# Optimization experiments

Measured on AMD Instinct MI355X. Metric: run time of the kernel, lower is better.

## Reference

```python
import jax, jax.numpy as jnp
import numpy as np

B, N, F, D, H, T = 32, 1024, 32, 64, 64, 4


def setup_inputs() -> dict:
    key = jax.random.key(0)
    ks = jax.random.split(key, 12)
    def w(k, shape):
        return 0.01 * jax.random.normal(k, shape, dtype=jnp.float32)
    z = lambda *s: jnp.zeros(s, jnp.float32)
    return {
        "xv": jax.random.normal(ks[0], (B, N, F), dtype=jnp.float32),
        "option": jax.random.uniform(ks[1], (B, 1), dtype=jnp.float32),
        "adj": jax.random.normal(ks[2], (N, N), dtype=jnp.float32),
        "mu1": w(ks[3], (F, D)),
        "W2": w(ks[4], (D, D)), "b2": z(D),
        "W3": w(ks[5], (D, D)), "b3": z(D),
        "W4": w(ks[6], (D, 1)), "b4": z(D),
        "Wq1": w(ks[7], (D, D)), "bq1": z(D),
        "Wq2": w(ks[8], (D, 1)), "bq2": z(D),
        "Wreg": w(ks[9], (H, 2 * D)), "breg": z(H),
        "Wq": w(ks[10], (1, H)), "bq": z(1),
    }


def reference(xv, option, adj, mu1, W2, b2, W3, b3, W4, b4,
              Wq1, bq1, Wq2, bq2, Wreg, breg, Wq, bq):
    # binary adjacency for message passing, raw weights for the mu_4 branch
    A = (adj > 0).astype(xv.dtype)                       # [N,N]
    mu_1 = jnp.maximum(xv @ mu1, 0.0)                    # [B,N,D]
    # mu_4: Linear(1,D) over every edge weight, clamp, sum over neighbors
    # (identical value every round t>=1, so computed once)
    mu4 = jnp.maximum(adj[..., None] * W4[:, 0] + b4, 0.0).sum(axis=1)[None]  # [1,N,D]
    mu3 = mu4 @ W3.T + b3                                # [1,N,D]
    mu = mu_1                                            # t = 0
    for _ in range(1, T):                                # t = 1..T-1
        mu_pool = jnp.einsum('nm,bmd->bnd', A, mu)       # neighbor aggregation
        mu2 = mu_pool @ W2.T + b2
        mu = jnp.maximum(mu_1 + mu2 + mu3, 0.0)
    mu_mean = jnp.maximum(mu.mean(axis=1, keepdims=True) @ Wq1.T + bq1, 0.0)  # [B,1,D]
    mu_aug = jnp.concatenate([mu, mu_mean], axis=1)      # [B,N+1,D]
    q2 = option.reshape(B, 1, 1) @ Wq2.T + bq2           # [B,1,D]
    q2 = jnp.broadcast_to(q2, (B, N + 1, D))
    q_ = jnp.concatenate([mu_aug, q2], axis=-1)          # [B,N+1,2D]
    qreg = jnp.maximum(q_ @ Wreg.T + breg, 0.0)          # [B,N+1,H]
    return qreg @ Wq.T + bq                              # [B,N+1,1]
```

## Files before the change

kernel.cpp:

```cpp
#include <hip/hip_runtime.h>
#include <hip/hip_bf16.h>

#define Bc 32
#define Nc 1024
#define Fc 32
#define Dc 64
#define Hc 64

typedef __bf16 bf16;
typedef __bf16 bf16x4 __attribute__((ext_vector_type(4)));
typedef __bf16 bf16x8 __attribute__((ext_vector_type(8)));
typedef float  f32x4  __attribute__((ext_vector_type(4)));

#define MS 72
#define LDS_RND_NONF 18432
#define LDS_RND_FIN  37376


__global__ void k_init(const float* __restrict__ adj, const float* __restrict__ W4,
                       const float* __restrict__ b4, const float* __restrict__ W3,
                       const float* __restrict__ b3, const float* __restrict__ b2,
                       const float* __restrict__ W2, const float* __restrict__ option,
                       const float* __restrict__ Wq2, const float* __restrict__ bq2,
                       const float* __restrict__ Wreg, const float* __restrict__ breg,
                       const float* __restrict__ xv, const float* __restrict__ mu1w,
                       bf16* __restrict__ Afrag, float* __restrict__ C3,
                       bf16* __restrict__ W2bf, float* __restrict__ c2base,
                       float* __restrict__ musum,
                       float* __restrict__ mu_1, bf16* __restrict__ Xfrag0) {
    const int id = blockIdx.x, t = threadIdx.x;
    __shared__ char smem[39424];
    if (id < 1024) {
        const int n = id;
        float* red   = (float*)smem;
        float* mu4_s = red + 256;
        const float* arow = adj + (size_t)n * Nc;
        {
            const int m0 = t * 4;
            const float4 a = *(const float4*)&arow[m0];
            bf16x4 o;
            o[0] = (bf16)((a.x > 0.f) ? 1.f : 0.f);
            o[1] = (bf16)((a.y > 0.f) ? 1.f : 0.f);
            o[2] = (bf16)((a.z > 0.f) ? 1.f : 0.f);
            o[3] = (bf16)((a.w > 0.f) ? 1.f : 0.f);
            const int g = n >> 4, lm = n & 15;
            const int k0 = m0 >> 5, q = (m0 & 31) >> 3, j = m0 & 7;
            *(bf16x4*)&Afrag[(size_t)((g * 32 + k0) * 64 + lm + 16 * q) * 8 + j] = o;
        }
        const int e = t & 63, g = t >> 6;
        const float w4e = W4[e], b4e = b4[e];
        float acc = 0.f;
        const float4* arow4 = (const float4*)(arow + g * 256);
#pragma unroll 8
        for (int j = 0; j < 64; ++j) {
            const float4 av = arow4[j];
            acc += fmaxf(fmaf(av.x, w4e, b4e), 0.f);
            acc += fmaxf(fmaf(av.y, w4e, b4e), 0.f);
            acc += fmaxf(fmaf(av.z, w4e, b4e), 0.f);
            acc += fmaxf(fmaf(av.w, w4e, b4e), 0.f);
        }
        red[t] = acc;
        __syncthreads();
        if (g == 0) mu4_s[e] = red[e] + red[64 + e] + red[128 + e] + red[192 + e];
        __syncthreads();
        if (t < 64) {
            const int d = t;
            float a = b3[d] + b2[d];
#pragma unroll
            for (int ee = 0; ee < 64; ++ee) a = fmaf(mu4_s[ee], W3[d * 64 + ee], a);
            C3[n * 64 + d] = a;
        }
    } else if (id == 1024) {
        for (int j = t * 16; j < t * 16 + 16; ++j) W2bf[j] = (bf16)W2[j];
        for (int i = t; i < 2048; i += 256) musum[i] = 0.f;
        for (int i = t; i < 2048; i += 256) {
            const int b = i >> 6, h = i & 63;
            const float opt = option[b];
            float a = breg[h];
#pragma unroll
            for (int j = 0; j < 64; ++j)
                a = fmaf(fmaf(opt, Wq2[j], bq2[j]), Wreg[h * 128 + 64 + j], a);
            c2base[i] = a;
        }
    } else {
        const int idx = id - 1025, nb = idx & 15, b = idx >> 4;
        const int n0 = nb * 64;
        const int l = t & 63, wv = t >> 6, lm = l & 15, q = l >> 4;
        bf16* W2s = (bf16*)smem;
        bf16* xhi = (bf16*)(smem + 9216);
        bf16* xlo = (bf16*)(smem + 14336);
        bf16* whi = (bf16*)(smem + 19456);
        bf16* wlo = (bf16*)(smem + 24576);
        bf16* muS = (bf16*)(smem + 29696);
        {
            const int row = t >> 2, f0 = (t & 3) * 8;
            const float* src = &xv[((size_t)b * Nc + n0 + row) * Fc + f0];
            const float4 v0 = *(const float4*)src;
            const float4 v1 = *(const float4*)(src + 4);
            bf16x8 hi, lo;
            float vv[8] = {v0.x, v0.y, v0.z, v0.w, v1.x, v1.y, v1.z, v1.w};
#pragma unroll
            for (int j = 0; j < 8; ++j) { hi[j] = (bf16)vv[j]; lo[j] = (bf16)(vv[j] - (float)hi[j]); }
            *(bf16x8*)&xhi[row * 40 + f0] = hi;
            *(bf16x8*)&xlo[row * 40 + f0] = lo;
        }
        {
            const int d = t >> 2, f0 = (t & 3) * 8;
#pragma unroll
            for (int j = 0; j < 8; ++j) {
                const float v = mu1w[(f0 + j) * Dc + d];
                const bf16 hi = (bf16)v;
                whi[d * 40 + f0 + j] = hi;
                wlo[d * 40 + f0 + j] = (bf16)(v - (float)hi);
            }
        }
        {
            const int row = t >> 2, c0 = (t & 3) * 16;
            const float4 v0 = *(const float4*)&W2[row * 64 + c0];
            const float4 v1 = *(const float4*)&W2[row * 64 + c0 + 4];
            const float4 v2 = *(const float4*)&W2[row * 64 + c0 + 8];
            const float4 v3 = *(const float4*)&W2[row * 64 + c0 + 12];
            bf16x8 p0, p1;
            p0[0]=(bf16)v0.x; p0[1]=(bf16)v0.y; p0[2]=(bf16)v0.z; p0[3]=(bf16)v0.w;
            p0[4]=(bf16)v1.x; p0[5]=(bf16)v1.y; p0[6]=(bf16)v1.z; p0[7]=(bf16)v1.w;
            p1[0]=(bf16)v2.x; p1[1]=(bf16)v2.y; p1[2]=(bf16)v2.z; p1[3]=(bf16)v2.w;
            p1[4]=(bf16)v3.x; p1[5]=(bf16)v3.y; p1[6]=(bf16)v3.z; p1[7]=(bf16)v3.w;
            *(bf16x8*)&W2s[row * MS + c0] = p0;
            *(bf16x8*)&W2s[row * MS + c0 + 8] = p1;
        }
        __syncthreads();
        f32x4 acc[4];
#pragma unroll
        for (int ct = 0; ct < 4; ++ct)
#pragma unroll
            for (int r = 0; r < 4; ++r) acc[ct][r] = 0.f;
        {
            const bf16x8 aHi = *(const bf16x8*)&xhi[(wv * 16 + lm) * 40 + q * 8];
            const bf16x8 aLo = *(const bf16x8*)&xlo[(wv * 16 + lm) * 40 + q * 8];
#pragma unroll
            for (int ct = 0; ct < 4; ++ct) {
                const bf16x8 bHi = *(const bf16x8*)&whi[(ct * 16 + lm) * 40 + q * 8];
                const bf16x8 bLo = *(const bf16x8*)&wlo[(ct * 16 + lm) * 40 + q * 8];
                acc[ct] = __builtin_amdgcn_mfma_f32_16x16x32_bf16(aHi, bHi, acc[ct], 0, 0, 0);
                acc[ct] = __builtin_amdgcn_mfma_f32_16x16x32_bf16(aLo, bHi, acc[ct], 0, 0, 0);
                acc[ct] = __builtin_amdgcn_mfma_f32_16x16x32_bf16(aHi, bLo, acc[ct], 0, 0, 0);
            }
        }
#pragma unroll
        for (int ct = 0; ct < 4; ++ct) {
            const int col = ct * 16 + lm;
#pragma unroll
            for (int r = 0; r < 4; ++r) {
                const int row = wv * 16 + q * 4 + r;
                const float v = fmaxf(acc[ct][r], 0.f);
                mu_1[((size_t)b * Nc + n0 + row) * Dc + col] = v;
                muS[row * MS + col] = (bf16)v;
            }
        }
        __syncthreads();
        f32x4 xacc[4];
#pragma unroll
        for (int ct = 0; ct < 4; ++ct)
#pragma unroll
            for (int r = 0; r < 4; ++r) xacc[ct][r] = 0.f;
#pragma unroll
        for (int s = 0; s < 2; ++s) {
            bf16x8 a = *(const bf16x8*)&muS[(wv * 16 + lm) * MS + s * 32 + q * 8];
#pragma unroll
            for (int ct = 0; ct < 4; ++ct) {
                bf16x8 bv = *(const bf16x8*)&W2s[(ct * 16 + lm) * MS + s * 32 + q * 8];
                xacc[ct] = __builtin_amdgcn_mfma_f32_16x16x32_bf16(a, bv, xacc[ct], 0, 0, 0);
            }
        }
        const int k0 = nb * 2 + (wv >> 1);
        const int q_c = (wv & 1) * 2 + (q >> 1);
        const int j0 = (q & 1) * 4;
#pragma unroll
        for (int ct = 0; ct < 4; ++ct) {
            bf16x4 p;
#pragma unroll
            for (int r = 0; r < 4; ++r) p[r] = (bf16)xacc[ct][r];
            *(bf16x4*)&Xfrag0[(size_t)b * 65536
                              + (size_t)((ct * 32 + k0) * 64 + lm + 16 * q_c) * 8 + j0] = p;
        }
    }
}

template <bool FINAL>
__global__ __launch_bounds__(256, 2)
void k_round(const bf16* __restrict__ Afrag, const bf16* __restrict__ Xfr_in,
             const float* __restrict__ mu_1, const float* __restrict__ C3,
             const bf16* __restrict__ W2bf, bf16* __restrict__ Xfr_out,
             const float* __restrict__ Wreg, const float* __restrict__ c2base,
             const float* __restrict__ Wq, const float* __restrict__ bq,
             float* __restrict__ musum, float* __restrict__ out) {
    const int b = blockIdx.x, nb = blockIdx.y, t = threadIdx.x;
    const int n0 = nb * 64;
    const int l = t & 63, wv = t >> 6, lm = l & 15, q = l >> 4;
    const int rh = wv & 1, ch = wv >> 1;
    extern __shared__ char smem[];
    bf16* muHi = (bf16*)smem;
    bf16* muLo = (bf16*)(smem + 9216);
    bf16* WHi  = (bf16*)(smem + (FINAL ? 18432 : 9216));
    bf16* WLo  = (bf16*)(smem + 27648);
    float* rpart = (float*)(smem + 36864);

    if (!FINAL) {
#pragma unroll
        for (int i = 0; i < 2; ++i) {
            int g = i * 256 + t, row = g >> 3, c = g & 7;
            *(bf16x8*)&WHi[row * MS + c * 8] = *(const bf16x8*)&W2bf[row * 64 + c * 8];
        }
    } else {
#pragma unroll
        for (int i = 0; i < 4; ++i) {
            int g = i * 1024 + t * 4, h = g >> 6, d = g & 63;
            const float4 w4 = *(const float4*)&Wreg[h * 128 + d];
            bf16x4 ohi, olo;
            ohi[0] = (bf16)w4.x; olo[0] = (bf16)(w4.x - (float)ohi[0]);
            ohi[1] = (bf16)w4.y; olo[1] = (bf16)(w4.y - (float)ohi[1]);
            ohi[2] = (bf16)w4.z; olo[2] = (bf16)(w4.z - (float)ohi[2]);
            ohi[3] = (bf16)w4.w; olo[3] = (bf16)(w4.w - (float)ohi[3]);
            *(bf16x4*)&WHi[h * MS + d] = ohi;
            *(bf16x4*)&WLo[h * MS + d] = olo;
        }
    }

    f32x4 acc[2][2];
#pragma unroll
    for (int rt = 0; rt < 2; ++rt)
#pragma unroll
        for (int ct = 0; ct < 2; ++ct)
#pragma unroll
            for (int r = 0; r < 4; ++r) acc[rt][ct][r] = 0.f;

    const int gA = nb * 4 + rh * 2;
    const bf16* pa0 = Afrag + (size_t)(gA + 0) * 32 * 512 + l * 8;
    const bf16* pa1 = Afrag + (size_t)(gA + 1) * 32 * 512 + l * 8;
    const bf16* px0 = Xfr_in + (size_t)b * 65536 + (size_t)(ch * 2 + 0) * 32 * 512 + l * 8;
    const bf16* px1 = Xfr_in + (size_t)b * 65536 + (size_t)(ch * 2 + 1) * 32 * 512 + l * 8;
#pragma unroll 4
    for (int k0 = 0; k0 < 32; ++k0) {
        const int o = k0 * 512;
        bf16x8 a0 = *(const bf16x8*)&pa0[o];
        bf16x8 a1 = *(const bf16x8*)&pa1[o];
        bf16x8 x0 = *(const bf16x8*)&px0[o];
        bf16x8 x1 = *(const bf16x8*)&px1[o];
        acc[0][0] = __builtin_amdgcn_mfma_f32_16x16x32_bf16(a0, x0, acc[0][0], 0, 0, 0);
        acc[0][1] = __builtin_amdgcn_mfma_f32_16x16x32_bf16(a0, x1, acc[0][1], 0, 0, 0);
        acc[1][0] = __builtin_amdgcn_mfma_f32_16x16x32_bf16(a1, x0, acc[1][0], 0, 0, 0);
        acc[1][1] = __builtin_amdgcn_mfma_f32_16x16x32_bf16(a1, x1, acc[1][1], 0, 0, 0);
    }

    float vals[2][2][4];
#pragma unroll
    for (int rt = 0; rt < 2; ++rt)
#pragma unroll
        for (int ct = 0; ct < 2; ++ct) {
            const int col = ch * 32 + ct * 16 + lm;
#pragma unroll
            for (int r = 0; r < 4; ++r) {
                const int n = n0 + rh * 32 + rt * 16 + q * 4 + r;
                float v = mu_1[((size_t)b * Nc + n) * Dc + col] + acc[rt][ct][r]
                        + C3[n * 64 + col];
                vals[rt][ct][r] = fmaxf(v, 0.f);
            }
        }

#pragma unroll
    for (int rt = 0; rt < 2; ++rt)
#pragma unroll
        for (int ct = 0; ct < 2; ++ct) {
            const int col = ch * 32 + ct * 16 + lm;
#pragma unroll
            for (int r = 0; r < 4; ++r) {
                const int row = rh * 32 + rt * 16 + q * 4 + r;
                const float v = vals[rt][ct][r];
                const bf16 hi = (bf16)v;
                muHi[row * MS + col] = hi;
                if (FINAL) muLo[row * MS + col] = (bf16)(v - (float)hi);
            }
        }
    if (FINAL) {
#pragma unroll
        for (int ct = 0; ct < 2; ++ct) {
            float s = 0.f;
#pragma unroll
            for (int rt = 0; rt < 2; ++rt)
#pragma unroll
                for (int r = 0; r < 4; ++r) s += vals[rt][ct][r];
            s += __shfl_xor(s, 16);
            s += __shfl_xor(s, 32);
            if (q == 0) atomicAdd(&musum[b * 64 + ch * 32 + ct * 16 + lm], s);
        }
    }
    __syncthreads();

    f32x4 xacc[2][2];
#pragma unroll
    for (int rt = 0; rt < 2; ++rt)
#pragma unroll
        for (int ct = 0; ct < 2; ++ct)
#pragma unroll
            for (int r = 0; r < 4; ++r) xacc[rt][ct][r] = 0.f;

    if (!FINAL) {
#pragma unroll
        for (int s = 0; s < 2; ++s) {
            bf16x8 aM[2], bW[2];
#pragma unroll
            for (int rt = 0; rt < 2; ++rt)
                aM[rt] = *(const bf16x8*)&muHi[(rh * 32 + rt * 16 + lm) * MS + s * 32 + q * 8];
#pragma unroll
            for (int ct = 0; ct < 2; ++ct)
                bW[ct] = *(const bf16x8*)&WHi[(ch * 32 + ct * 16 + lm) * MS + s * 32 + q * 8];
#pragma unroll
            for (int rt = 0; rt < 2; ++rt)
#pragma unroll
                for (int ct = 0; ct < 2; ++ct)
                    xacc[rt][ct] = __builtin_amdgcn_mfma_f32_16x16x32_bf16(aM[rt], bW[ct],
                                                                           xacc[rt][ct], 0, 0, 0);
        }
        const int k0 = nb * 2 + rh;
        const int q_c0 = (q >> 1), j0 = (q & 1) * 4;
#pragma unroll
        for (int rt = 0; rt < 2; ++rt)
#pragma unroll
            for (int ct = 0; ct < 2; ++ct) {
                bf16x4 p;
#pragma unroll
                for (int r = 0; r < 4; ++r) p[r] = (bf16)xacc[rt][ct][r];
                *(bf16x4*)&Xfr_out[(size_t)b * 65536
                    + (size_t)(((ch * 2 + ct) * 32 + k0) * 64 + lm + 16 * (rt * 2 + q_c0)) * 8
                    + j0] = p;
            }
    } else {
#pragma unroll
        for (int s = 0; s < 2; ++s) {
            bf16x8 aH[2], aL[2], bH[2], bL[2];
#pragma unroll
            for (int rt = 0; rt < 2; ++rt) {
                const int ao = (rh * 32 + rt * 16 + lm) * MS + s * 32 + q * 8;
                aH[rt] = *(const bf16x8*)&muHi[ao];
                aL[rt] = *(const bf16x8*)&muLo[ao];
            }
#pragma unroll
            for (int ct = 0; ct < 2; ++ct) {
                const int bo = (ch * 32 + ct * 16 + lm) * MS + s * 32 + q * 8;
                bH[ct] = *(const bf16x8*)&WHi[bo];
                bL[ct] = *(const bf16x8*)&WLo[bo];
            }
#pragma unroll
            for (int rt = 0; rt < 2; ++rt)
#pragma unroll
                for (int ct = 0; ct < 2; ++ct) {
                    xacc[rt][ct] = __builtin_amdgcn_mfma_f32_16x16x32_bf16(aH[rt], bH[ct],
                                                                           xacc[rt][ct], 0, 0, 0);
                    xacc[rt][ct] = __builtin_amdgcn_mfma_f32_16x16x32_bf16(aL[rt], bH[ct],
                                                                           xacc[rt][ct], 0, 0, 0);
                    xacc[rt][ct] = __builtin_amdgcn_mfma_f32_16x16x32_bf16(aH[rt], bL[ct],
                                                                           xacc[rt][ct], 0, 0, 0);
                }
        }
        const float bq0 = bq[0];
        float rowsum[2][4] = {{0.f, 0.f, 0.f, 0.f}, {0.f, 0.f, 0.f, 0.f}};
#pragma unroll
        for (int ct = 0; ct < 2; ++ct) {
            const int h = ch * 32 + ct * 16 + lm;
            const float c2 = c2base[b * 64 + h];
            const float wqh = Wq[h];
#pragma unroll
            for (int rt = 0; rt < 2; ++rt)
#pragma unroll
                for (int r = 0; r < 4; ++r)
                    rowsum[rt][r] += fmaxf(xacc[rt][ct][r] + c2, 0.f) * wqh;
        }
#pragma unroll
        for (int rt = 0; rt < 2; ++rt)
#pragma unroll
            for (int r = 0; r < 4; ++r) {
                float v = rowsum[rt][r];
                v += __shfl_xor(v, 1);
                v += __shfl_xor(v, 2);
                v += __shfl_xor(v, 4);
                v += __shfl_xor(v, 8);
                if (lm == 0) rpart[ch * 64 + rh * 32 + rt * 16 + q * 4 + r] = v;
            }
        __syncthreads();
        if (t < 64)
            out[(size_t)b * (Nc + 1) + n0 + t] = rpart[t] + rpart[64 + t] + bq0;
    }
}

__global__ void k_tail(const float* __restrict__ musum, const float* __restrict__ Wq1,
                       const float* __restrict__ bq1, const float* __restrict__ Wreg,
                       const float* __restrict__ c2base, const float* __restrict__ Wq,
                       const float* __restrict__ bq, float* __restrict__ out) {
    const int b = blockIdx.x, l = threadIdx.x;
    __shared__ float mean_s[64];
    __shared__ float mp[64];
    mean_s[l] = musum[b * 64 + l] * (1.f / Nc);
    __syncthreads();
    float a = bq1[l];
#pragma unroll
    for (int e = 0; e < 64; ++e) a = fmaf(mean_s[e], Wq1[l * 64 + e], a);
    mp[l] = fmaxf(a, 0.f);
    __syncthreads();
    float h = c2base[b * 64 + l];
#pragma unroll
    for (int d = 0; d < 64; ++d) h = fmaf(mp[d], Wreg[l * 128 + d], h);
    float v = fmaxf(h, 0.f) * Wq[l];
#pragma unroll
    for (int off = 32; off; off >>= 1) v += __shfl_down(v, off);
    if (l == 0) out[(size_t)b * (Nc + 1) + Nc] = v + bq[0];
}

extern "C" void kernel_launch(void* const* d_in, const int* in_sizes, int n_in,
                              void* d_out, int out_size, void* d_ws, size_t ws_size,
                              hipStream_t stream) {
    const float* xv     = (const float*)d_in[0];
    const float* option = (const float*)d_in[1];
    const float* adj    = (const float*)d_in[2];
    const float* mu1w   = (const float*)d_in[3];
    const float* W2     = (const float*)d_in[4];
    const float* b2     = (const float*)d_in[5];
    const float* W3     = (const float*)d_in[6];
    const float* b3     = (const float*)d_in[7];
    const float* W4     = (const float*)d_in[8];
    const float* b4     = (const float*)d_in[9];
    const float* Wq1    = (const float*)d_in[10];
    const float* bq1    = (const float*)d_in[11];
    const float* Wq2    = (const float*)d_in[12];
    const float* bq2    = (const float*)d_in[13];
    const float* Wreg   = (const float*)d_in[14];
    const float* breg   = (const float*)d_in[15];
    const float* Wq     = (const float*)d_in[16];
    const float* bq     = (const float*)d_in[17];
    float* out = (float*)d_out;

    float* ws = (float*)d_ws;
    const size_t MU = (size_t)Bc * Nc * Dc;
    float* mu_1     = ws;
    float* C3       = ws + MU;
    float* c2base   = C3 + 65536;
    float* musum    = c2base + 2048;
    bf16*  Afrag    = (bf16*)(musum + 2048);
    bf16*  W2bf     = Afrag + (size_t)Nc * Nc;
    bf16*  Xf0      = W2bf + 4096;
    bf16*  Xf1      = Xf0 + MU;

    k_init<<<1537, 256, 0, stream>>>(adj, W4, b4, W3, b3, b2, W2, option, Wq2, bq2,
                                     Wreg, breg, xv, mu1w,
                                     Afrag, C3, W2bf, c2base, musum, mu_1, Xf0);
    k_round<false><<<dim3(Bc, 16), 256, LDS_RND_NONF, stream>>>(
        Afrag, Xf0, mu_1, C3, W2bf, Xf1,
        nullptr, nullptr, nullptr, nullptr, nullptr, nullptr);
    k_round<false><<<dim3(Bc, 16), 256, LDS_RND_NONF, stream>>>(
        Afrag, Xf1, mu_1, C3, W2bf, Xf0,
        nullptr, nullptr, nullptr, nullptr, nullptr, nullptr);
    k_round<true><<<dim3(Bc, 16), 256, LDS_RND_FIN, stream>>>(
        Afrag, Xf0, mu_1, C3, nullptr, nullptr,
        Wreg, c2base, Wq, bq, musum, out);
    k_tail<<<Bc, 64, 0, stream>>>(musum, Wq1, bq1, Wreg, c2base, Wq, bq, out);
}
```

Baseline: 153.0 us.

## Double-buffer MFMA operand loads and fold tail into final round via ticket

The k-loop of the round kernel now prefetches the next group of four A/X fragments into registers while running MFMAs on the current group. The mu_1 and C3 epilogue operands are loaded before the loop so their latency is hidden. The separate tail kernel is removed: the last block per batch, chosen by an atomic ticket counter, computes the mean-path output. This saves a launch, but it raises register pressure under launch bounds and relies on threadfence/atomic ordering.

Result: slower. 184.4 us (+20.5%).

```diff
diff --git a/kernel.cpp b/kernel.cpp
--- a/kernel.cpp
+++ b/kernel.cpp
@@ -26,7 +26,7 @@
                        const float* __restrict__ xv, const float* __restrict__ mu1w,
                        bf16* __restrict__ Afrag, float* __restrict__ C3,
                        bf16* __restrict__ W2bf, float* __restrict__ c2base,
-                       float* __restrict__ musum,
+                       float* __restrict__ musum, int* __restrict__ ticket,
                        float* __restrict__ mu_1, bf16* __restrict__ Xfrag0) {
     const int id = blockIdx.x, t = threadIdx.x;
     __shared__ char smem[39424];
@@ -73,6 +73,7 @@
     } else if (id == 1024) {
         for (int j = t * 16; j < t * 16 + 16; ++j) W2bf[j] = (bf16)W2[j];
         for (int i = t; i < 2048; i += 256) musum[i] = 0.f;
+        if (t < 32) ticket[t] = 0;
         for (int i = t; i < 2048; i += 256) {
             const int b = i >> 6, h = i & 63;
             const float opt = option[b];
@@ -193,7 +194,9 @@
              const bf16* __restrict__ W2bf, bf16* __restrict__ Xfr_out,
              const float* __restrict__ Wreg, const float* __restrict__ c2base,
              const float* __restrict__ Wq, const float* __restrict__ bq,
-             float* __restrict__ musum, float* __restrict__ out) {
+             const float* __restrict__ Wq1, const float* __restrict__ bq1,
+             float* __restrict__ musum, int* __restrict__ ticket,
+             float* __restrict__ out) {
     const int b = blockIdx.x, nb = blockIdx.y, t = threadIdx.x;
     const int n0 = nb * 64;
     const int l = t & 63, wv = t >> 6, lm = l & 15, q = l >> 4;
@@ -239,20 +242,17 @@
     const bf16* pa1 = Afrag + (size_t)(gA + 1) * 32 * 512 + l * 8;
     const bf16* px0 = Xfr_in + (size_t)b * 65536 + (size_t)(ch * 2 + 0) * 32 * 512 + l * 8;
     const bf16* px1 = Xfr_in + (size_t)b * 65536 + (size_t)(ch * 2 + 1) * 32 * 512 + l * 8;
-#pragma unroll 4
-    for (int k0 = 0; k0 < 32; ++k0) {
-        const int o = k0 * 512;
-        bf16x8 a0 = *(const bf16x8*)&pa0[o];
-        bf16x8 a1 = *(const bf16x8*)&pa1[o];
-        bf16x8 x0 = *(const bf16x8*)&px0[o];
-        bf16x8 x1 = *(const bf16x8*)&px1[o];
-        acc[0][0] = __builtin_amdgcn_mfma_f32_16x16x32_bf16(a0, x0, acc[0][0], 0, 0, 0);
-        acc[0][1] = __builtin_amdgcn_mfma_f32_16x16x32_bf16(a0, x1, acc[0][1], 0, 0, 0);
-        acc[1][0] = __builtin_amdgcn_mfma_f32_16x16x32_bf16(a1, x0, acc[1][0], 0, 0, 0);
-        acc[1][1] = __builtin_amdgcn_mfma_f32_16x16x32_bf16(a1, x1, acc[1][1], 0, 0, 0);
+
+    bf16x8 bA0[2][4], bA1[2][4], bX0[2][4], bX1[2][4];
+#pragma unroll
+    for (int i = 0; i < 4; ++i) {
+        const int o = i * 512;
+        bA0[0][i] = *(const bf16x8*)&pa0[o];
+        bA1[0][i] = *(const bf16x8*)&pa1[o];
+        bX0[0][i] = *(const bf16x8*)&px0[o];
+        bX1[0][i] = *(const bf16x8*)&px1[o];
     }
-
-    float vals[2][2][4];
+    float pmu[2][2][4], pc3[2][2][4];
 #pragma unroll
     for (int rt = 0; rt < 2; ++rt)
 #pragma unroll
@@ -261,11 +261,42 @@
 #pragma unroll
             for (int r = 0; r < 4; ++r) {
                 const int n = n0 + rh * 32 + rt * 16 + q * 4 + r;
-                float v = mu_1[((size_t)b * Nc + n) * Dc + col] + acc[rt][ct][r]
-                        + C3[n * 64 + col];
-                vals[rt][ct][r] = fmaxf(v, 0.f);
-            }
-        }
+                pmu[rt][ct][r] = mu_1[((size_t)b * Nc + n) * Dc + col];
+                pc3[rt][ct][r] = C3[n * 64 + col];
+            }
+        }
+
+#pragma unroll
+    for (int g = 0; g < 8; ++g) {
+        const int cur = g & 1, nxt = cur ^ 1;
+        if (g < 7) {
+            const int o0 = (g + 1) * 4 * 512;
+#pragma unroll
+            for (int i = 0; i < 4; ++i) {
+                const int o = o0 + i * 512;
+                bA0[nxt][i] = *(const bf16x8*)&pa0[o];
+                bA1[nxt][i] = *(const bf16x8*)&pa1[o];
+                bX0[nxt][i] = *(const bf16x8*)&px0[o];
+                bX1[nxt][i] = *(const bf16x8*)&px1[o];
+            }
+        }
+#pragma unroll
+        for (int i = 0; i < 4; ++i) {
+            acc[0][0] = __builtin_amdgcn_mfma_f32_16x16x32_bf16(bA0[cur][i], bX0[cur][i], acc[0][0], 0, 0, 0);
+            acc[0][1] = __builtin_amdgcn_mfma_f32_16x16x32_bf16(bA0[cur][i], bX1[cur][i], acc[0][1], 0, 0, 0);
+            acc[1][0] = __builtin_amdgcn_mfma_f32_16x16x32_bf16(bA1[cur][i], bX0[cur][i], acc[1][0], 0, 0, 0);
+            acc[1][1] = __builtin_amdgcn_mfma_f32_16x16x32_bf16(bA1[cur][i], bX1[cur][i], acc[1][1], 0, 0, 0);
+        }
+    }
+
+    float vals[2][2][4];
+#pragma unroll
+    for (int rt = 0; rt < 2; ++rt)
+#pragma unroll
+        for (int ct = 0; ct < 2; ++ct)
+#pragma unroll
+            for (int r = 0; r < 4; ++r)
+                vals[rt][ct][r] = fmaxf(pmu[rt][ct][r] + acc[rt][ct][r] + pc3[rt][ct][r], 0.f);
 
 #pragma unroll
     for (int rt = 0; rt < 2; ++rt)
@@ -389,30 +420,34 @@
         __syncthreads();
         if (t < 64)
             out[(size_t)b * (Nc + 1) + n0 + t] = rpart[t] + rpart[64 + t] + bq0;
+
+        __threadfence();
+        __shared__ int lastFlag;
+        if (t == 0) lastFlag = (atomicAdd(&ticket[b], 1) == 15) ? 1 : 0;
+        __syncthreads();
+        if (lastFlag) {
+            float* mean_s = (float*)smem;
+            float* mp     = mean_s + 64;
+            if (t < 64) mean_s[t] = atomicAdd(&musum[b * 64 + t], 0.f) * (1.f / Nc);
+            __syncthreads();
+            if (t < 64) {
+                float a = bq1[t];
+#pragma unroll
+                for (int e = 0; e < 64; ++e) a = fmaf(mean_s[e], Wq1[t * 64 + e], a);
+                mp[t] = fmaxf(a, 0.f);
+            }
+            __syncthreads();
+            if (t < 64) {
+                float h = c2base[b * 64 + t];
+#pragma unroll
+                for (int d = 0; d < 64; ++d) h = fmaf(mp[d], Wreg[t * 128 + d], h);
+                float v = fmaxf(h, 0.f) * Wq[t];
+#pragma unroll
+                for (int off = 32; off; off >>= 1) v += __shfl_down(v, off);
+                if (t == 0) out[(size_t)b * (Nc + 1) + Nc] = v + bq0;
+            }
+        }
     }
-}
-
-__global__ void k_tail(const float* __restrict__ musum, const float* __restrict__ Wq1,
-                       const float* __restrict__ bq1, const float* __restrict__ Wreg,
-                       const float* __restrict__ c2base, const float* __restrict__ Wq,
-                       const float* __restrict__ bq, float* __restrict__ out) {
-    const int b = blockIdx.x, l = threadIdx.x;
-    __shared__ float mean_s[64];
-    __shared__ float mp[64];
-    mean_s[l] = musum[b * 64 + l] * (1.f / Nc);
-    __syncthreads();
-    float a = bq1[l];
-#pragma unroll
-    for (int e = 0; e < 64; ++e) a = fmaf(mean_s[e], Wq1[l * 64 + e], a);
-    mp[l] = fmaxf(a, 0.f);
-    __syncthreads();
-    float h = c2base[b * 64 + l];
-#pragma unroll
-    for (int d = 0; d < 64; ++d) h = fmaf(mp[d], Wreg[l * 128 + d], h);
-    float v = fmaxf(h, 0.f) * Wq[l];
-#pragma unroll
-    for (int off = 32; off; off >>= 1) v += __shfl_down(v, off);
-    if (l == 0) out[(size_t)b * (Nc + 1) + Nc] = v + bq[0];
 }
 
 extern "C" void kernel_launch(void* const* d_in, const int* in_sizes, int n_in,
@@ -444,22 +479,22 @@
     float* C3       = ws + MU;
     float* c2base   = C3 + 65536;
     float* musum    = c2base + 2048;
-    bf16*  Afrag    = (bf16*)(musum + 2048);
+    int*   ticket   = (int*)(musum + 2048);
+    bf16*  Afrag    = (bf16*)(ticket + 64);
     bf16*  W2bf     = Afrag + (size_t)Nc * Nc;
     bf16*  Xf0      = W2bf + 4096;
     bf16*  Xf1      = Xf0 + MU;
 
     k_init<<<1537, 256, 0, stream>>>(adj, W4, b4, W3, b3, b2, W2, option, Wq2, bq2,
                                      Wreg, breg, xv, mu1w,
-                                     Afrag, C3, W2bf, c2base, musum, mu_1, Xf0);
+                                     Afrag, C3, W2bf, c2base, musum, ticket, mu_1, Xf0);
     k_round<false><<<dim3(Bc, 16), 256, LDS_RND_NONF, stream>>>(
         Afrag, Xf0, mu_1, C3, W2bf, Xf1,
-        nullptr, nullptr, nullptr, nullptr, nullptr, nullptr);
+        nullptr, nullptr, nullptr, nullptr, nullptr, nullptr, nullptr, nullptr, nullptr);
     k_round<false><<<dim3(Bc, 16), 256, LDS_RND_NONF, stream>>>(
         Afrag, Xf1, mu_1, C3, W2bf, Xf0,
-        nullptr, nullptr, nullptr, nullptr, nullptr, nullptr);
+        nullptr, nullptr, nullptr, nullptr, nullptr, nullptr, nullptr, nullptr, nullptr);
     k_round<true><<<dim3(Bc, 16), 256, LDS_RND_FIN, stream>>>(
         Afrag, Xf0, mu_1, C3, nullptr, nullptr,
-        Wreg, c2base, Wq, bq, musum, out);
-    k_tail<<<Bc, 64, 0, stream>>>(musum, Wq1, bq1, Wreg, c2base, Wq, bq, out);
+        Wreg, c2base, Wq, bq, Wq1, bq1, musum, ticket, out);
 }
```

## Halve row tile per block in round kernel to double grid and occupancy

Applied to the files above, without the earlier changes.

Each round block now handles 32 node rows instead of 64, so the grid doubles to 32x32 blocks and each wave computes a single 16-row tile. The aim is to fill more CUs and raise occupancy (launch bounds raised to 4 blocks per SM, smaller LDS). mu_1 and C3 epilogue operands are prefetched before the aggregation loop so their latency overlaps with the MFMAs. In exchange, the per-block MFMA work drops and the X fragments are reloaded from memory by twice as many blocks, which adds global/L2 traffic.

Result: slower. 159.8 us (+4.5%).

```diff
diff --git a/kernel.cpp b/kernel.cpp
--- a/kernel.cpp
+++ b/kernel.cpp
@@ -13,8 +13,8 @@
 typedef float  f32x4  __attribute__((ext_vector_type(4)));
 
 #define MS 72
-#define LDS_RND_NONF 18432
-#define LDS_RND_FIN  37376
+#define LDS_RND_NONF 13824
+#define LDS_RND_FIN  27904
 
 
 __global__ void k_init(const float* __restrict__ adj, const float* __restrict__ W4,
@@ -187,7 +187,7 @@
 }
 
 template <bool FINAL>
-__global__ __launch_bounds__(256, 2)
+__global__ __launch_bounds__(256, 4)
 void k_round(const bf16* __restrict__ Afrag, const bf16* __restrict__ Xfr_in,
              const float* __restrict__ mu_1, const float* __restrict__ C3,
              const bf16* __restrict__ W2bf, bf16* __restrict__ Xfr_out,
@@ -195,15 +195,15 @@
              const float* __restrict__ Wq, const float* __restrict__ bq,
              float* __restrict__ musum, float* __restrict__ out) {
     const int b = blockIdx.x, nb = blockIdx.y, t = threadIdx.x;
-    const int n0 = nb * 64;
+    const int n0 = nb * 32;
     const int l = t & 63, wv = t >> 6, lm = l & 15, q = l >> 4;
     const int rh = wv & 1, ch = wv >> 1;
     extern __shared__ char smem[];
     bf16* muHi = (bf16*)smem;
-    bf16* muLo = (bf16*)(smem + 9216);
-    bf16* WHi  = (bf16*)(smem + (FINAL ? 18432 : 9216));
-    bf16* WLo  = (bf16*)(smem + 27648);
-    float* rpart = (float*)(smem + 36864);
+    bf16* muLo = (bf16*)(smem + 4608);
+    bf16* WHi  = (bf16*)(smem + (FINAL ? 9216 : 4608));
+    bf16* WLo  = (bf16*)(smem + 18432);
+    float* rpart = (float*)(smem + 27648);
 
     if (!FINAL) {
 #pragma unroll
@@ -226,69 +226,62 @@
         }
     }
 
-    f32x4 acc[2][2];
-#pragma unroll
-    for (int rt = 0; rt < 2; ++rt)
-#pragma unroll
-        for (int ct = 0; ct < 2; ++ct)
-#pragma unroll
-            for (int r = 0; r < 4; ++r) acc[rt][ct][r] = 0.f;
-
-    const int gA = nb * 4 + rh * 2;
-    const bf16* pa0 = Afrag + (size_t)(gA + 0) * 32 * 512 + l * 8;
-    const bf16* pa1 = Afrag + (size_t)(gA + 1) * 32 * 512 + l * 8;
+    f32x4 acc[2];
+#pragma unroll
+    for (int ct = 0; ct < 2; ++ct)
+#pragma unroll
+        for (int r = 0; r < 4; ++r) acc[ct][r] = 0.f;
+
+    const int gA = nb * 2 + rh;
+    const bf16* pa  = Afrag + (size_t)gA * 32 * 512 + l * 8;
     const bf16* px0 = Xfr_in + (size_t)b * 65536 + (size_t)(ch * 2 + 0) * 32 * 512 + l * 8;
     const bf16* px1 = Xfr_in + (size_t)b * 65536 + (size_t)(ch * 2 + 1) * 32 * 512 + l * 8;
-#pragma unroll 4
+
+    float pmu[2][4], pc3[2][4];
+#pragma unroll
+    for (int ct = 0; ct < 2; ++ct) {
+        const int col = ch * 32 + ct * 16 + lm;
+#pragma unroll
+        for (int r = 0; r < 4; ++r) {
+            const int n = n0 + rh * 16 + q * 4 + r;
+            pmu[ct][r] = mu_1[((size_t)b * Nc + n) * Dc + col];
+            pc3[ct][r] = C3[n * 64 + col];
+        }
+    }
+
+#pragma unroll 8
     for (int k0 = 0; k0 < 32; ++k0) {
         const int o = k0 * 512;
-        bf16x8 a0 = *(const bf16x8*)&pa0[o];
-        bf16x8 a1 = *(const bf16x8*)&pa1[o];
+        bf16x8 a  = *(const bf16x8*)&pa[o];
         bf16x8 x0 = *(const bf16x8*)&px0[o];
         bf16x8 x1 = *(const bf16x8*)&px1[o];
-        acc[0][0] = __builtin_amdgcn_mfma_f32_16x16x32_bf16(a0, x0, acc[0][0], 0, 0, 0);
-        acc[0][1] = __builtin_amdgcn_mfma_f32_16x16x32_bf16(a0, x1, acc[0][1], 0, 0, 0);
-        acc[1][0] = __builtin_amdgcn_mfma_f32_16x16x32_bf16(a1, x0, acc[1][0], 0, 0, 0);
-        acc[1][1] = __builtin_amdgcn_mfma_f32_16x16x32_bf16(a1, x1, acc[1][1], 0, 0, 0);
-    }
-
-    float vals[2][2][4];
-#pragma unroll
-    for (int rt = 0; rt < 2; ++rt)
+        acc[0] = __builtin_amdgcn_mfma_f32_16x16x32_bf16(a, x0, acc[0], 0, 0, 0);
+        acc[1] = __builtin_amdgcn_mfma_f32_16x16x32_bf16(a, x1, acc[1], 0, 0, 0);
+    }
+
+    float vals[2][4];
+#pragma unroll
+    for (int ct = 0; ct < 2; ++ct)
+#pragma unroll
+        for (int r = 0; r < 4; ++r)
+            vals[ct][r] = fmaxf(pmu[ct][r] + acc[ct][r] + pc3[ct][r], 0.f);
+
+#pragma unroll
+    for (int ct = 0; ct < 2; ++ct) {
+        const int col = ch * 32 + ct * 16 + lm;
+#pragma unroll
+        for (int r = 0; r < 4; ++r) {
+            const int row = rh * 16 + q * 4 + r;
+            const float v = vals[ct][r];
+            const bf16 hi = (bf16)v;
+            muHi[row * MS + col] = hi;
+            if (FINAL) muLo[row * MS + col] = (bf16)(v - (float)hi);
+        }
+    }
+    if (FINAL) {
 #pragma unroll
         for (int ct = 0; ct < 2; ++ct) {
-            const int col = ch * 32 + ct * 16 + lm;
-#pragma unroll
-            for (int r = 0; r < 4; ++r) {
-                const int n = n0 + rh * 32 + rt * 16 + q * 4 + r;
-                float v = mu_1[((size_t)b * Nc + n) * Dc + col] + acc[rt][ct][r]
-                        + C3[n * 64 + col];
-                vals[rt][ct][r] = fmaxf(v, 0.f);
-            }
-        }
-
-#pragma unroll
-    for (int rt = 0; rt < 2; ++rt)
-#pragma unroll
-        for (int ct = 0; ct < 2; ++ct) {
-            const int col = ch * 32 + ct * 16 + lm;
-#pragma unroll
-            for (int r = 0; r < 4; ++r) {
-                const int row = rh * 32 + rt * 16 + q * 4 + r;
-                const float v = vals[rt][ct][r];
-                const bf16 hi = (bf16)v;
-                muHi[row * MS + col] = hi;
-                if (FINAL) muLo[row * MS + col] = (bf16)(v - (float)hi);
-            }
-        }
-    if (FINAL) {
-#pragma unroll
-        for (int ct = 0; ct < 2; ++ct) {
-            float s = 0.f;
-#pragma unroll
-            for (int rt = 0; rt < 2; ++rt)
-#pragma unroll
-                for (int r = 0; r < 4; ++r) s += vals[rt][ct][r];
+            float s = vals[ct][0] + vals[ct][1] + vals[ct][2] + vals[ct][3];
             s += __shfl_xor(s, 16);
             s += __shfl_xor(s, 32);
             if (q == 0) atomicAdd(&musum[b * 64 + ch * 32 + ct * 16 + lm], s);
@@ -296,99 +289,70 @@
     }
     __syncthreads();
 
-    f32x4 xacc[2][2];
-#pragma unroll
-    for (int rt = 0; rt < 2; ++rt)
-#pragma unroll
-        for (int ct = 0; ct < 2; ++ct)
-#pragma unroll
-            for (int r = 0; r < 4; ++r) xacc[rt][ct][r] = 0.f;
+    f32x4 xacc[2];
+#pragma unroll
+    for (int ct = 0; ct < 2; ++ct)
+#pragma unroll
+        for (int r = 0; r < 4; ++r) xacc[ct][r] = 0.f;
 
     if (!FINAL) {
 #pragma unroll
         for (int s = 0; s < 2; ++s) {
-            bf16x8 aM[2], bW[2];
-#pragma unroll
-            for (int rt = 0; rt < 2; ++rt)
-                aM[rt] = *(const bf16x8*)&muHi[(rh * 32 + rt * 16 + lm) * MS + s * 32 + q * 8];
-#pragma unroll
-            for (int ct = 0; ct < 2; ++ct)
-                bW[ct] = *(const bf16x8*)&WHi[(ch * 32 + ct * 16 + lm) * MS + s * 32 + q * 8];
-#pragma unroll
-            for (int rt = 0; rt < 2; ++rt)
-#pragma unroll
-                for (int ct = 0; ct < 2; ++ct)
-                    xacc[rt][ct] = __builtin_amdgcn_mfma_f32_16x16x32_bf16(aM[rt], bW[ct],
-                                                                           xacc[rt][ct], 0, 0, 0);
-        }
-        const int k0 = nb * 2 + rh;
-        const int q_c0 = (q >> 1), j0 = (q & 1) * 4;
-#pragma unroll
-        for (int rt = 0; rt < 2; ++rt)
+            bf16x8 a = *(const bf16x8*)&muHi[(rh * 16 + lm) * MS + s * 32 + q * 8];
 #pragma unroll
             for (int ct = 0; ct < 2; ++ct) {
-                bf16x4 p;
-#pragma unroll
-                for (int r = 0; r < 4; ++r) p[r] = (bf16)xacc[rt][ct][r];
-                *(bf16x4*)&Xfr_out[(size_t)b * 65536
-                    + (size_t)(((ch * 2 + ct) * 32 + k0) * 64 + lm + 16 * (rt * 2 + q_c0)) * 8
-                    + j0] = p;
-            }
+                bf16x8 bv = *(const bf16x8*)&WHi[(ch * 32 + ct * 16 + lm) * MS + s * 32 + q * 8];
+                xacc[ct] = __builtin_amdgcn_mfma_f32_16x16x32_bf16(a, bv, xacc[ct], 0, 0, 0);
+            }
+        }
+        const int q_c = rh * 2 + (q >> 1), j0 = (q & 1) * 4;
+#pragma unroll
+        for (int ct = 0; ct < 2; ++ct) {
+            bf16x4 p;
+#pragma unroll
+            for (int r = 0; r < 4; ++r) p[r] = (bf16)xacc[ct][r];
+            *(bf16x4*)&Xfr_out[(size_t)b * 65536
+                + (size_t)(((ch * 2 + ct) * 32 + nb) * 64 + lm + 16 * q_c) * 8 + j0] = p;
+        }
     } else {
 #pragma unroll
         for (int s = 0; s < 2; ++s) {
-            bf16x8 aH[2], aL[2], bH[2], bL[2];
-#pragma unroll
-            for (int rt = 0; rt < 2; ++rt) {
-                const int ao = (rh * 32 + rt * 16 + lm) * MS + s * 32 + q * 8;
-                aH[rt] = *(const bf16x8*)&muHi[ao];
-                aL[rt] = *(const bf16x8*)&muLo[ao];
-            }
+            const int ao = (rh * 16 + lm) * MS + s * 32 + q * 8;
+            bf16x8 aH = *(const bf16x8*)&muHi[ao];
+            bf16x8 aL = *(const bf16x8*)&muLo[ao];
 #pragma unroll
             for (int ct = 0; ct < 2; ++ct) {
                 const int bo = (ch * 32 + ct * 16 + lm) * MS + s * 32 + q * 8;
-                bH[ct] = *(const bf16x8*)&WHi[bo];
-                bL[ct] = *(const bf16x8*)&WLo[bo];
-            }
-#pragma unroll
-            for (int rt = 0; rt < 2; ++rt)
-#pragma unroll
-                for (int ct = 0; ct < 2; ++ct) {
-                    xacc[rt][ct] = __builtin_amdgcn_mfma_f32_16x16x32_bf16(aH[rt], bH[ct],
-                                                                           xacc[rt][ct], 0, 0, 0);
-                    xacc[rt][ct] = __builtin_amdgcn_mfma_f32_16x16x32_bf16(aL[rt], bH[ct],
-                                                                           xacc[rt][ct], 0, 0, 0);
-                    xacc[rt][ct] = __builtin_amdgcn_mfma_f32_16x16x32_bf16(aH[rt], bL[ct],
-                                                                           xacc[rt][ct], 0, 0, 0);
-                }
+                bf16x8 bH = *(const bf16x8*)&WHi[bo];
+                bf16x8 bL = *(const bf16x8*)&WLo[bo];
+                xacc[ct] = __builtin_amdgcn_mfma_f32_16x16x32_bf16(aH, bH, xacc[ct], 0, 0, 0);
+                xacc[ct] = __builtin_amdgcn_mfma_f32_16x16x32_bf16(aL, bH, xacc[ct], 0, 0, 0);
+                xacc[ct] = __builtin_amdgcn_mfma_f32_16x16x32_bf16(aH, bL, xacc[ct], 0, 0, 0);
+            }
         }
         const float bq0 = bq[0];
-        float rowsum[2][4] = {{0.f, 0.f, 0.f, 0.f}, {0.f, 0.f, 0.f, 0.f}};
+        float rowsum[4] = {0.f, 0.f, 0.f, 0.f};
 #pragma unroll
         for (int ct = 0; ct < 2; ++ct) {
             const int h = ch * 32 + ct * 16 + lm;
             const float c2 = c2base[b * 64 + h];
             const float wqh = Wq[h];
 #pragma unroll
-            for (int rt = 0; rt < 2; ++rt)
-#pragma unroll
-                for (int r = 0; r < 4; ++r)
-                    rowsum[rt][r] += fmaxf(xacc[rt][ct][r] + c2, 0.f) * wqh;
-        }
-#pragma unroll
-        for (int rt = 0; rt < 2; ++rt)
-#pragma unroll
-            for (int r = 0; r < 4; ++r) {
-                float v = rowsum[rt][r];
-                v += __shfl_xor(v, 1);
-                v += __shfl_xor(v, 2);
-                v += __shfl_xor(v, 4);
-                v += __shfl_xor(v, 8);
-                if (lm == 0) rpart[ch * 64 + rh * 32 + rt * 16 + q * 4 + r] = v;
-            }
+            for (int r = 0; r < 4; ++r)
+                rowsum[r] += fmaxf(xacc[ct][r] + c2, 0.f) * wqh;
+        }
+#pragma unroll
+        for (int r = 0; r < 4; ++r) {
+            float v = rowsum[r];
+            v += __shfl_xor(v, 1);
+            v += __shfl_xor(v, 2);
+            v += __shfl_xor(v, 4);
+            v += __shfl_xor(v, 8);
+            if (lm == 0) rpart[ch * 32 + rh * 16 + q * 4 + r] = v;
+        }
         __syncthreads();
-        if (t < 64)
-            out[(size_t)b * (Nc + 1) + n0 + t] = rpart[t] + rpart[64 + t] + bq0;
+        if (t < 32)
+            out[(size_t)b * (Nc + 1) + n0 + t] = rpart[t] + rpart[32 + t] + bq0;
     }
 }
 
@@ -452,13 +416,13 @@
     k_init<<<1537, 256, 0, stream>>>(adj, W4, b4, W3, b3, b2, W2, option, Wq2, bq2,
                                      Wreg, breg, xv, mu1w,
                                      Afrag, C3, W2bf, c2base, musum, mu_1, Xf0);
-    k_round<false><<<dim3(Bc, 16), 256, LDS_RND_NONF, stream>>>(
+    k_round<false><<<dim3(Bc, 32), 256, LDS_RND_NONF, stream>>>(
         Afrag, Xf0, mu_1, C3, W2bf, Xf1,
         nullptr, nullptr, nullptr, nullptr, nullptr, nullptr);
-    k_round<false><<<dim3(Bc, 16), 256, LDS_RND_NONF, stream>>>(
+    k_round<false><<<dim3(Bc, 32), 256, LDS_RND_NONF, stream>>>(
         Afrag, Xf1, mu_1, C3, W2bf, Xf0,
         nullptr, nullptr, nullptr, nullptr, nullptr, nullptr);
-    k_round<true><<<dim3(Bc, 16), 256, LDS_RND_FIN, stream>>>(
+    k_round<true><<<dim3(Bc, 32), 256, LDS_RND_FIN, stream>>>(
         Afrag, Xf0, mu_1, C3, nullptr, nullptr,
         Wreg, c2base, Wq, bq, musum, out);
     k_tail<<<Bc, 64, 0, stream>>>(musum, Wq1, bq1, Wreg, c2base, Wq, bq, out);
```
